# Kernel tuning notes

Hardware: AMD Instinct MI355X
Metric: run time of the kernel (lower is better)

Reference implementation:

```python
import jax, jax.numpy as jnp
import numpy as np

N_NODES = 4096
IN_FEAT = 256
N_HEADS = 8
N_HIDDEN = 32  # out_features // n_heads
NEG_SLOPE = 0.2


def setup_inputs() -> dict:
    key = jax.random.key(0)
    k1, k2, k3, k4 = jax.random.split(key, 4)
    h = jax.random.normal(k1, (N_NODES, IN_FEAT), dtype=jnp.float32)
    W = jax.random.normal(k2, (N_HEADS * N_HIDDEN, IN_FEAT), dtype=jnp.float32) * 0.05
    a = jax.random.normal(k3, (2 * N_HIDDEN,), dtype=jnp.float32) * 0.05
    adj_mat = jax.random.randint(k4, (N_NODES, N_NODES, 1), 0, 2, dtype=jnp.int32)
    return {"h": h, "W": W, "a": a, "adj_mat": adj_mat}


def reference(h, W, a, adj_mat):
    n = h.shape[0]
    # g = linear(h) -> [N, H, F]
    g = (h @ W.T).reshape(n, N_HEADS, N_HIDDEN)
    # e_ij = LeakyReLU(a^T [g_i || g_j]) = LeakyReLU(a_l . g_i + a_r . g_j)
    a_l, a_r = a[:N_HIDDEN], a[N_HIDDEN:]
    s_i = jnp.einsum('nhf,f->nh', g, a_l)  # destination term (repeat_interleave axis)
    s_j = jnp.einsum('nhf,f->nh', g, a_r)  # source term (repeat axis)
    e = jax.nn.leaky_relu(s_i[:, None, :] + s_j[None, :, :], NEG_SLOPE)  # [N, N, H]
    e = jnp.where(adj_mat == 0, jnp.float32(-jnp.inf), e)
    att = jax.nn.softmax(e, axis=1)  # softmax over source nodes j
    # dropout(p) in eval mode -> identity
    out = jnp.einsum('ijh,jhf->ihf', att, g)
    return out.reshape(n, N_HEADS * N_HIDDEN)  # is_concat=True
```

## Files before the change

### kernel.cpp

```cpp
#include <hip/hip_runtime.h>
#include <math.h>

constexpr int N   = 4096;
constexpr int F   = 256;
constexpr int NH  = 8;
constexpr int HID = 32;
constexpr float SLOPE = 0.2f;

using h2       = __attribute__((ext_vector_type(2))) _Float16;
using frag_f16 = __attribute__((ext_vector_type(8))) _Float16;
using frag_cd  = __attribute__((ext_vector_type(4))) float;
using frag_c16 = __attribute__((ext_vector_type(16))) float;

__device__ inline unsigned short f2h(float x) {
  _Float16 v = (_Float16)x;
  unsigned short u; __builtin_memcpy(&u, &v, 2); return u;
}

__global__ __launch_bounds__(256) void k_u(const float* __restrict__ W,
                                           const float* __restrict__ a,
                                           float* __restrict__ U) {
  const int c = blockIdx.x, k = threadIdx.x;
  const int head = c & 7, side = c >> 3;
  float acc = 0.f;
#pragma unroll
  for (int f = 0; f < 32; ++f)
    acc += W[(size_t)(head * 32 + f) * F + k] * a[side * 32 + f];
  U[c * F + k] = acc;
}

__global__ __launch_bounds__(256) void k_front(const float* __restrict__ h,
                                               const float* __restrict__ W,
                                               const float* __restrict__ U,
                                               const int* __restrict__ adj,
                                               unsigned int* __restrict__ RT2,
                                               unsigned short* __restrict__ BT,
                                               unsigned short* __restrict__ DT,
                                               unsigned short* __restrict__ gT,
                                               unsigned int* __restrict__ bits) {
  const int b = blockIdx.x, t = threadIdx.x;
  if (b < 256) {
    const int i0 = b * 16;
    const int r = t >> 4, c = t & 15;
    const float4* hp = (const float4*)(h + (size_t)(i0 + r) * F);
    const float4* up = (const float4*)(U + (size_t)c * F);
    float acc = 0.f;
#pragma unroll
    for (int k4 = 0; k4 < 64; ++k4) {
      const float4 hv = hp[k4];
      const float4 uv = up[k4];
      acc += hv.x * uv.x + hv.y * uv.y + hv.z * uv.z + hv.w * uv.w;
    }
    const int n = i0 + r;
    if (c < 8) {
      const unsigned int r16 = f2h(__expf(-0.8f * acc));
      RT2[(size_t)n * NH + c] = (r16 << 16) | r16;
    } else {
      const int hd = c - 8;
      BT[(size_t)hd * N + n] = f2h(__expf(acc));
      DT[(size_t)hd * N + n] = f2h(__expf(SLOPE * acc));
    }
  } else if (b < 1280) {
    const int lane = t & 63;
    const int tile = (b - 256) * 4 + (t >> 6);
    const int mt = tile >> 4, nt = tile & 15;
    const int m0 = mt * 16, n0 = nt * 16;
    const int n16 = lane & 15, quad = lane >> 4;
    frag_cd acc = {0.f, 0.f, 0.f, 0.f};
    const float* ap = h + (size_t)(m0 + n16) * F + quad * 8;
    const float* bp = W + (size_t)(n0 + n16) * F + quad * 8;
#pragma unroll
    for (int ks = 0; ks < F / 32; ++ks) {
      const float4 a0 = *(const float4*)(ap + ks * 32);
      const float4 a1 = *(const float4*)(ap + ks * 32 + 4);
      const float4 b0 = *(const float4*)(bp + ks * 32);
      const float4 b1 = *(const float4*)(bp + ks * 32 + 4);
      const frag_f16 af = {(_Float16)a0.x, (_Float16)a0.y, (_Float16)a0.z, (_Float16)a0.w,
                           (_Float16)a1.x, (_Float16)a1.y, (_Float16)a1.z, (_Float16)a1.w};
      const frag_f16 bf = {(_Float16)b0.x, (_Float16)b0.y, (_Float16)b0.z, (_Float16)b0.w,
                           (_Float16)b1.x, (_Float16)b1.y, (_Float16)b1.z, (_Float16)b1.w};
      acc = __builtin_amdgcn_mfma_f32_16x16x32_f16(af, bf, acc, 0, 0, 0);
    }
    unsigned short tmp[4];
#pragma unroll
    for (int reg = 0; reg < 4; ++reg) tmp[reg] = f2h(acc[reg]);
    *(int2*)(gT + (size_t)(n0 + n16) * N + m0 + quad * 4) = *(int2*)tmp;
  } else {
    const int lane = t & 63;
    const int wv   = t >> 6;
    const int row  = (b - 1280) * 2 + (wv >> 1);
    const int half = wv & 1;
    const int4* src4 = (const int4*)(adj + (size_t)row * N) + half * 512 + lane;
    const int shamt = (lane & 7) * 4;
    unsigned int* dstw = bits + (size_t)row * (N / 32) + half * 64 + (lane >> 3);
#pragma unroll
    for (int it = 0; it < 8; ++it) {
      const int4 v4 = src4[it * 64];
      unsigned int v = ((unsigned)v4.x | ((unsigned)v4.y << 1) |
                        ((unsigned)v4.z << 2) | ((unsigned)v4.w << 3)) << shamt;
      v |= (unsigned)__shfl_xor((int)v, 1);
      v |= (unsigned)__shfl_xor((int)v, 2);
      v |= (unsigned)__shfl_xor((int)v, 4);
      if ((lane & 7) == 0) dstw[it * 8] = v;
    }
  }
}

constexpr int TI = 64;
constexpr int NSPLIT = 4;

__global__ __launch_bounds__(256, 4) void k_agg(
    const unsigned short* __restrict__ gT,
    const unsigned int* __restrict__ RT2,
    const unsigned short* __restrict__ BT, const unsigned short* __restrict__ DT,
    const unsigned int* __restrict__ bits,
    float* __restrict__ parts, float* __restrict__ lparts) {
  __shared__ __align__(16) unsigned short sB[64][140];
  __shared__ __align__(16) uint4 sBD[2][2][128];

  const int t    = threadIdx.x;
  const int lane = t & 63;
  const int wv   = t >> 6;
  const int isub = wv & 1;
  const int hd   = wv >> 1;
  const int b    = blockIdx.x;
  const int hp   = b & 3;
  const int js   = (b >> 2) & (NSPLIT - 1);
  const int i0   = (b >> 4) * TI;
  const int head = hp * 2 + hd;

  const int n32 = lane & 31;
  const int kh  = lane >> 5;

  const int myi = i0 + isub * 32 + n32;
  const unsigned int Ri2u = RT2[(size_t)myi * NH + head];
  h2 Ri2; __builtin_memcpy(&Ri2, &Ri2u, 4);
  const uint4* bp4 = (const uint4*)(bits + (size_t)myi * (N / 32) + js * 32);

  frag_c16 acc = {0.f, 0.f, 0.f, 0.f, 0.f, 0.f, 0.f, 0.f,
                  0.f, 0.f, 0.f, 0.f, 0.f, 0.f, 0.f, 0.f};
  frag_c16 accl = {0.f, 0.f, 0.f, 0.f, 0.f, 0.f, 0.f, 0.f,
                   0.f, 0.f, 0.f, 0.f, 0.f, 0.f, 0.f, 0.f};
  frag_f16 fone;
#pragma unroll
  for (int u = 0; u < 8; ++u) fone[u] = (_Float16)1.0f;

  const int sr = t >> 2, ss0 = t & 3;
  const unsigned short* gsrc = gT + (size_t)(hp * 64 + sr) * N + js * 1024;

  {
    const int hsel = t >> 7, idx = t & 127;
    sBD[0][hsel][idx] =
        ((const uint4*)(BT + (size_t)(hp * 2 + hsel) * N + js * 1024))[idx];
    sBD[1][hsel][idx] =
        ((const uint4*)(DT + (size_t)(hp * 2 + hsel) * N + js * 1024))[idx];
  }
  {
    int4 pre[4];
#pragma unroll
    for (int s = 0; s < 4; ++s)
      pre[s] = *(const int4*)(gsrc + (ss0 + s * 4) * 8);
#pragma unroll
    for (int s = 0; s < 4; ++s) {
      const int seg = ss0 + s * 4;
      *(int2*)&sB[sr][seg * 8]     = make_int2(pre[s].x, pre[s].y);
      *(int2*)&sB[sr][seg * 8 + 4] = make_int2(pre[s].z, pre[s].w);
    }
  }
  __syncthreads();

  uint4 bw = bp4[0];
  for (int c8 = 0; c8 < 8; ++c8) {
    const uint4 bwn = (c8 < 7) ? bp4[c8 + 1] : bw;
    int4 nxt[4];
    if (c8 < 7) {
#pragma unroll
      for (int s = 0; s < 4; ++s)
        nxt[s] = *(const int4*)(gsrc + (c8 + 1) * 128 + (ss0 + s * 4) * 8);
    }
    const unsigned int bwa[4] = {bw.x, bw.y, bw.z, bw.w};
#pragma unroll
    for (int half = 0; half < 2; ++half) {
      uint4 Bva[4], Dva[4];
#pragma unroll
      for (int q = 0; q < 4; ++q) {
        const int ss = half * 4 + q;
        Bva[q] = sBD[0][hd][c8 * 16 + ss * 2 + kh];
        Dva[q] = sBD[1][hd][c8 * 16 + ss * 2 + kh];
      }
#pragma unroll
      for (int q = 0; q < 4; ++q) {
        const int ss = half * 4 + q;
        const int jb = ss * 16 + kh * 8;
        const unsigned int mb = (bwa[ss >> 1] >> (((ss & 1) << 4) + (kh << 3))) & 0xFFu;
        const unsigned int bu[4] = {Bva[q].x, Bva[q].y, Bva[q].z, Bva[q].w};
        const unsigned int du[4] = {Dva[q].x, Dva[q].y, Dva[q].z, Dva[q].w};
        unsigned int packed[4];
#pragma unroll
        for (int p = 0; p < 4; ++p) {
          h2 hB, hD;
          __builtin_memcpy(&hB, &bu[p], 4);
          __builtin_memcpy(&hD, &du[p], 4);
          const h2 wm = __builtin_elementwise_max(hB, Ri2 * hD);
          unsigned int wp; __builtin_memcpy(&wp, &wm, 4);
          const unsigned int d  = (mb >> (2 * p)) & 3u;
          const unsigned int sp = ((d | (d << 15)) & 0x10001u) * 0xFFFFu;
          wp &= sp;
          packed[p] = wp;
        }
        frag_f16 af; __builtin_memcpy(&af, packed, 16);

        const int frow = hd * 32 + n32;
        const int2 blo = *(const int2*)&sB[frow][jb];
        const int2 bhi = *(const int2*)&sB[frow][jb + 4];
        const int bt[4] = {blo.x, blo.y, bhi.x, bhi.y};
        frag_f16 bf; __builtin_memcpy(&bf, bt, 16);

        acc  = __builtin_amdgcn_mfma_f32_32x32x16_f16(af, bf, acc, 0, 0, 0);
        accl = __builtin_amdgcn_mfma_f32_32x32x16_f16(af, fone, accl, 0, 0, 0);
      }
    }
    if (c8 < 7) {
      __syncthreads();
#pragma unroll
      for (int s = 0; s < 4; ++s) {
        const int seg = ss0 + s * 4;
        *(int2*)&sB[sr][seg * 8]     = make_int2(nxt[s].x, nxt[s].y);
        *(int2*)&sB[sr][seg * 8 + 4] = make_int2(nxt[s].z, nxt[s].w);
      }
      __syncthreads();
    }
    bw = bwn;
  }

  float* op = parts + (size_t)js * N * F;
#pragma unroll
  for (int reg = 0; reg < 16; ++reg) {
    const int row = (reg & 3) + 8 * (reg >> 2) + 4 * kh;
    op[(size_t)(i0 + isub * 32 + row) * F + head * HID + n32] = acc[reg];
  }
  if (n32 == 0) {
    float* lp = lparts + (size_t)js * N * NH;
#pragma unroll
    for (int reg = 0; reg < 16; ++reg) {
      const int row = (reg & 3) + 8 * (reg >> 2) + 4 * kh;
      lp[(size_t)(i0 + isub * 32 + row) * NH + head] = accl[reg];
    }
  }
}

__global__ __launch_bounds__(256) void k_norm(const float* __restrict__ parts,
                                              const float* __restrict__ lparts,
                                              float* __restrict__ out) {
  const int idx = blockIdx.x * 256 + threadIdx.x;
  const int i = idx >> 6, fq = idx & 63;
  const int hh = fq >> 3;
  float l = 0.f;
  float4 v = make_float4(0.f, 0.f, 0.f, 0.f);
#pragma unroll
  for (int js = 0; js < NSPLIT; ++js) {
    l += lparts[(size_t)js * N * NH + (size_t)i * NH + hh];
    const float4 p = *(const float4*)(parts + (size_t)js * N * F + (size_t)idx * 4);
    v.x += p.x; v.y += p.y; v.z += p.z; v.w += p.w;
  }
  const float inv = 1.f / l;
  v.x *= inv; v.y *= inv; v.z *= inv; v.w *= inv;
  *(float4*)(out + (size_t)idx * 4) = v;
}

extern "C" void kernel_launch(void* const* d_in, const int* in_sizes, int n_in,
                              void* d_out, int out_size, void* d_ws, size_t ws_size,
                              hipStream_t stream) {
  const float* h   = (const float*)d_in[0];
  const float* W   = (const float*)d_in[1];
  const float* a   = (const float*)d_in[2];
  const int*   adj = (const int*)d_in[3];
  float* out = (float*)d_out;

  char* ws = (char*)d_ws;
  unsigned short* gT = (unsigned short*)ws;  ws += (size_t)N * F * 2;
  unsigned int* bits = (unsigned int*)ws;    ws += (size_t)N * (N / 32) * 4;
  unsigned int* RT2 = (unsigned int*)ws;     ws += (size_t)N * NH * 4;
  unsigned short* BT = (unsigned short*)ws;  ws += (size_t)N * NH * 2;
  unsigned short* DT = (unsigned short*)ws;  ws += (size_t)N * NH * 2;
  float* U    = (float*)ws;                  ws += 16 * F * 4;
  float* parts  = (float*)ws;                ws += (size_t)NSPLIT * N * F * 4;
  float* lparts = (float*)ws;                ws += (size_t)NSPLIT * N * NH * 4;

  k_u<<<dim3(16), dim3(256), 0, stream>>>(W, a, U);
  k_front<<<dim3(3328), dim3(256), 0, stream>>>(h, W, U, adj, RT2, BT, DT, gT, bits);
  k_agg<<<dim3((N / TI) * 4 * NSPLIT), dim3(256), 0, stream>>>(
      gT, RT2, BT, DT, bits, parts, lparts);
  k_norm<<<dim3(N * F / 4 / 256), dim3(256), 0, stream>>>(parts, lparts, out);
}
```

Before: 156.6 us.

## Store g in MFMA fragment order and load B operands directly into registers

The projection kernel now writes g into a pre-swizzled layout that matches the 32x32x16 MFMA B-fragment lane order. The aggregation kernel then loads each fragment with one contiguous 16-byte global load per lane. This removes the shared-memory staging buffer and the two per-iteration block barriers. The next chunk's fragments are prefetched into registers, which raises register use and may affect occupancy; each wave also now reads its head's g data from global/L2 on its own instead of sharing it through LDS.

```diff
diff --git a/kernel.cpp b/kernel.cpp
--- a/kernel.cpp
+++ b/kernel.cpp
@@ -36,7 +36,7 @@
                                                unsigned int* __restrict__ RT2,
                                                unsigned short* __restrict__ BT,
                                                unsigned short* __restrict__ DT,
-                                               unsigned short* __restrict__ gT,
+                                               unsigned short* __restrict__ gT2,
                                                unsigned int* __restrict__ bits) {
   const int b = blockIdx.x, t = threadIdx.x;
   if (b < 256) {
@@ -84,7 +84,14 @@
     unsigned short tmp[4];
 #pragma unroll
     for (int reg = 0; reg < 4; ++reg) tmp[reg] = f2h(acc[reg]);
-    *(int2*)(gT + (size_t)(n0 + n16) * N + m0 + quad * 4) = *(int2*)tmp;
+    const int r  = n0 + n16;
+    const int m  = m0 + quad * 4;
+    const int head_ = r >> 5, n32_ = r & 31;
+    const int js_ = m >> 10, c8_ = (m >> 7) & 7, ss_ = (m >> 4) & 7;
+    const int kh_ = (m >> 3) & 1, e_ = m & 7;
+    unsigned short* dst = gT2 + ((size_t)(head_ * 4 + js_) * 64 + (c8_ * 8 + ss_)) * 512
+                              + (kh_ * 32 + n32_) * 8 + e_;
+    *(int2*)dst = *(int2*)tmp;
   } else {
     const int lane = t & 63;
     const int wv   = t >> 6;
@@ -110,12 +117,11 @@
 constexpr int NSPLIT = 4;
 
 __global__ __launch_bounds__(256, 4) void k_agg(
-    const unsigned short* __restrict__ gT,
+    const unsigned short* __restrict__ gT2,
     const unsigned int* __restrict__ RT2,
     const unsigned short* __restrict__ BT, const unsigned short* __restrict__ DT,
     const unsigned int* __restrict__ bits,
     float* __restrict__ parts, float* __restrict__ lparts) {
-  __shared__ __align__(16) unsigned short sB[64][140];
   __shared__ __align__(16) uint4 sBD[2][2][128];
 
   const int t    = threadIdx.x;
@@ -137,6 +143,9 @@
   h2 Ri2; __builtin_memcpy(&Ri2, &Ri2u, 4);
   const uint4* bp4 = (const uint4*)(bits + (size_t)myi * (N / 32) + js * 32);
 
+  const unsigned short* gfrag =
+      gT2 + (size_t)(head * NSPLIT + js) * 32768 + (size_t)lane * 8;
+
   frag_c16 acc = {0.f, 0.f, 0.f, 0.f, 0.f, 0.f, 0.f, 0.f,
                   0.f, 0.f, 0.f, 0.f, 0.f, 0.f, 0.f, 0.f};
   frag_c16 accl = {0.f, 0.f, 0.f, 0.f, 0.f, 0.f, 0.f, 0.f,
@@ -144,9 +153,6 @@
   frag_f16 fone;
 #pragma unroll
   for (int u = 0; u < 8; ++u) fone[u] = (_Float16)1.0f;
-
-  const int sr = t >> 2, ss0 = t & 3;
-  const unsigned short* gsrc = gT + (size_t)(hp * 64 + sr) * N + js * 1024;
 
   {
     const int hsel = t >> 7, idx = t & 127;
@@ -155,28 +161,22 @@
     sBD[1][hsel][idx] =
         ((const uint4*)(DT + (size_t)(hp * 2 + hsel) * N + js * 1024))[idx];
   }
-  {
-    int4 pre[4];
-#pragma unroll
-    for (int s = 0; s < 4; ++s)
-      pre[s] = *(const int4*)(gsrc + (ss0 + s * 4) * 8);
-#pragma unroll
-    for (int s = 0; s < 4; ++s) {
-      const int seg = ss0 + s * 4;
-      *(int2*)&sB[sr][seg * 8]     = make_int2(pre[s].x, pre[s].y);
-      *(int2*)&sB[sr][seg * 8 + 4] = make_int2(pre[s].z, pre[s].w);
-    }
-  }
   __syncthreads();
 
+  int4 bva[8];
+#pragma unroll
+  for (int ss = 0; ss < 8; ++ss)
+    bva[ss] = *(const int4*)(gfrag + (size_t)ss * 512);
   uint4 bw = bp4[0];
+
   for (int c8 = 0; c8 < 8; ++c8) {
-    const uint4 bwn = (c8 < 7) ? bp4[c8 + 1] : bw;
-    int4 nxt[4];
+    int4 nba[8];
+    uint4 bwn = bw;
     if (c8 < 7) {
-#pragma unroll
-      for (int s = 0; s < 4; ++s)
-        nxt[s] = *(const int4*)(gsrc + (c8 + 1) * 128 + (ss0 + s * 4) * 8);
+      bwn = bp4[c8 + 1];
+#pragma unroll
+      for (int ss = 0; ss < 8; ++ss)
+        nba[ss] = *(const int4*)(gfrag + (size_t)((c8 + 1) * 8 + ss) * 512);
     }
     const unsigned int bwa[4] = {bw.x, bw.y, bw.z, bw.w};
 #pragma unroll
@@ -191,7 +191,6 @@
 #pragma unroll
       for (int q = 0; q < 4; ++q) {
         const int ss = half * 4 + q;
-        const int jb = ss * 16 + kh * 8;
         const unsigned int mb = (bwa[ss >> 1] >> (((ss & 1) << 4) + (kh << 3))) & 0xFFu;
         const unsigned int bu[4] = {Bva[q].x, Bva[q].y, Bva[q].z, Bva[q].w};
         const unsigned int du[4] = {Dva[q].x, Dva[q].y, Dva[q].z, Dva[q].w};
@@ -209,28 +208,17 @@
           packed[p] = wp;
         }
         frag_f16 af; __builtin_memcpy(&af, packed, 16);
-
-        const int frow = hd * 32 + n32;
-        const int2 blo = *(const int2*)&sB[frow][jb];
-        const int2 bhi = *(const int2*)&sB[frow][jb + 4];
-        const int bt[4] = {blo.x, blo.y, bhi.x, bhi.y};
-        frag_f16 bf; __builtin_memcpy(&bf, bt, 16);
+        frag_f16 bf; __builtin_memcpy(&bf, &bva[ss], 16);
 
         acc  = __builtin_amdgcn_mfma_f32_32x32x16_f16(af, bf, acc, 0, 0, 0);
         accl = __builtin_amdgcn_mfma_f32_32x32x16_f16(af, fone, accl, 0, 0, 0);
       }
     }
     if (c8 < 7) {
-      __syncthreads();
-#pragma unroll
-      for (int s = 0; s < 4; ++s) {
-        const int seg = ss0 + s * 4;
-        *(int2*)&sB[sr][seg * 8]     = make_int2(nxt[s].x, nxt[s].y);
-        *(int2*)&sB[sr][seg * 8 + 4] = make_int2(nxt[s].z, nxt[s].w);
-      }
-      __syncthreads();
-    }
-    bw = bwn;
+#pragma unroll
+      for (int ss = 0; ss < 8; ++ss) bva[ss] = nba[ss];
+      bw = bwn;
+    }
   }
 
   float* op = parts + (size_t)js * N * F;
@@ -278,7 +266,7 @@
   float* out = (float*)d_out;
 
   char* ws = (char*)d_ws;
-  unsigned short* gT = (unsigned short*)ws;  ws += (size_t)N * F * 2;
+  unsigned short* gT2 = (unsigned short*)ws; ws += (size_t)N * F * 2;
   unsigned int* bits = (unsigned int*)ws;    ws += (size_t)N * (N / 32) * 4;
   unsigned int* RT2 = (unsigned int*)ws;     ws += (size_t)N * NH * 4;
   unsigned short* BT = (unsigned short*)ws;  ws += (size_t)N * NH * 2;
@@ -288,8 +276,8 @@
   float* lparts = (float*)ws;                ws += (size_t)NSPLIT * N * NH * 4;
 
   k_u<<<dim3(16), dim3(256), 0, stream>>>(W, a, U);
-  k_front<<<dim3(3328), dim3(256), 0, stream>>>(h, W, U, adj, RT2, BT, DT, gT, bits);
+  k_front<<<dim3(3328), dim3(256), 0, stream>>>(h, W, U, adj, RT2, BT, DT, gT2, bits);
   k_agg<<<dim3((N / TI) * 4 * NSPLIT), dim3(256), 0, stream>>>(
-      gT, RT2, BT, DT, bits, parts, lparts);
+      gT2, RT2, BT, DT, bits, parts, lparts);
   k_norm<<<dim3(N * F / 4 / 256), dim3(256), 0, stream>>>(parts, lparts, out);
 }
```

Result: faster. 152.1 us (-2.9%).
